# Optimization experiments

Hardware: AMD Instinct MI355X
Metric: run time of the kernel (lower is better)

Reference implementation:

```python
import jax, jax.numpy as jnp
import numpy as np

B, N, C, D = 4, 8192, 256, 256
WS = [2048, 4096, 8192]
RS = [1, 2, 4]
HEAD_IDX = 0


def setup_inputs() -> dict:
    key = jax.random.key(0)
    k1, k2, k3, k4 = jax.random.split(key, 4)
    scale = 1.0 / np.sqrt(C).astype(np.float32)
    x = jax.random.normal(k1, (B, N, C), jnp.float32)
    Wq = jax.random.normal(k2, (C, D), jnp.float32) * scale
    Wk = jax.random.normal(k3, (C, D), jnp.float32) * scale
    Wv = jax.random.normal(k4, (C, D), jnp.float32) * scale
    return {"x": x, "Wq": Wq, "Wk": Wk, "Wv": Wv}


def _causal_attn(v, Wq, Wk, Wv):
    # v: [Bseg, m, c] -> out [Bseg, m, D], denom [Bseg, m] (= sum_k exp(score))
    q = v @ Wq
    k = v @ Wk
    val = v @ Wv
    scores = jnp.einsum('bqd,bkd->bqk', q, k) / jnp.sqrt(jnp.asarray(D, v.dtype))
    m = v.shape[1]
    mask = jnp.tril(jnp.ones((m, m), bool))
    scores = jnp.where(mask, scores, -jnp.inf)
    mx = scores.max(-1)  # diagonal always unmasked -> finite
    e = jnp.exp(scores - mx[..., None])
    ssum = e.sum(-1)
    out = jnp.einsum('bqk,bkd->bqd', e, val) / ssum[..., None]
    denom = ssum * jnp.exp(mx)  # unnormalized softmax denominator
    return out, denom


def _dilated_forward(x, Wq, Wk, Wv):
    b, n, c = x.shape
    segs, idx_list = [], []
    for w, r in zip(WS, RS):
        off = HEAD_IDX % r
        s_cnt = n // w
        # [b, s, m, c] strided gather (offset::r within each window of size w)
        xr = x.reshape(b, s_cnt, w, c)[:, :, off::r, :]
        # segment-major then batch, matching torch.cat(..., dim=0) order
        segs.append(jnp.transpose(xr, (1, 0, 2, 3)).reshape(s_cnt * b, -1, c))
        pos = jnp.arange(off, w, r)
        idx_list.append(jnp.arange(s_cnt)[:, None] * w + pos[None, :])  # [s, m]
    batched = jnp.concatenate(segs, 0)  # [28, 2048, c]
    o_b, den_b = _causal_attn(batched, Wq, Wk, Wv)

    # per-token denominator sums across overlapping segments (scatter-add)
    sums = jnp.zeros((b, n), x.dtype)
    per_cfg = []
    start = 0
    for (w, r), idx in zip(zip(WS, RS), idx_list):
        s_cnt = n // w
        cnt = s_cnt * b
        o = jnp.transpose(o_b[start:start + cnt].reshape(s_cnt, b, -1, D), (1, 0, 2, 3))
        d = jnp.transpose(den_b[start:start + cnt].reshape(s_cnt, b, -1), (1, 0, 2))
        start += cnt
        flat_idx = idx.reshape(-1)  # [s*m]
        o_f = o.reshape(b, -1, D)
        d_f = d.reshape(b, -1)
        per_cfg.append((o_f, d_f, flat_idx))
        sums = sums.at[:, flat_idx].add(d_f)

    # weighted scatter-add of outputs, alpha = denom / denom_sum
    out = jnp.zeros((b, n, D), x.dtype)
    for o_f, d_f, flat_idx in per_cfg:
        alphas = d_f / sums[:, flat_idx]
        out = out.at[:, flat_idx, :].add(o_f * alphas[..., None])
    return out


def reference(x, Wq, Wk, Wv):
    return _dilated_forward(x, Wq, Wk, Wv)
```

## Files before the change

### kernel.cpp

```cpp
#include <hip/hip_runtime.h>
#include <hip/hip_bf16.h>

typedef __bf16 bf16;
typedef unsigned short u16;
typedef bf16 bf16x8 __attribute__((ext_vector_type(8)));
typedef bf16 bf16x2 __attribute__((ext_vector_type(2)));
typedef u16  u16x8  __attribute__((ext_vector_type(8)));
typedef u16  u16x4  __attribute__((ext_vector_type(4)));
typedef float f32x4 __attribute__((ext_vector_type(4)));
typedef float f32x16 __attribute__((ext_vector_type(16)));

#define MFMA16(a,b,c) __builtin_amdgcn_mfma_f32_16x16x32_bf16((a),(b),(c),0,0,0)
#define MFMA32(a,b,c) __builtin_amdgcn_mfma_f32_32x32x16_bf16((a),(b),(c),0,0,0)
#define QSCALE 0.09016844005625f

__device__ inline unsigned pack2(float a, float b) {
    bf16x2 t; t[0] = (bf16)a; t[1] = (bf16)b;
    return __builtin_bit_cast(unsigned, t);
}

__device__ __forceinline__ void load_lds16(const void* g, void* l) {
    __builtin_amdgcn_global_load_lds(
        (const __attribute__((address_space(1))) unsigned*)g,
        (__attribute__((address_space(3))) unsigned*)l, 16, 0, 0);
}

__device__ const unsigned short g_items[24] = {
    (unsigned short)(15 | (0u<<4) | (32u<<5)),
    (unsigned short)(14 | (0u<<4) | (32u<<5)),
    (unsigned short)(13 | (0u<<4) | (32u<<5)),
    (unsigned short)(12 | (0u<<4) | (32u<<5)),
    (unsigned short)(11 | (0u<<4) | (32u<<5)),
    (unsigned short)(10 | (0u<<4) | (32u<<5)),
    (unsigned short)( 9 | (0u<<4) | (32u<<5)),
    (unsigned short)( 8 | (0u<<4) | (32u<<5)),
    (unsigned short)(15 | (1u<<4) | (64u<<5)),
    (unsigned short)( 7 | (0u<<4) | (32u<<5)),
    (unsigned short)(14 | (1u<<4) | (60u<<5)),
    (unsigned short)( 6 | (0u<<4) | (28u<<5)),
    (unsigned short)(13 | (1u<<4) | (56u<<5)),
    (unsigned short)( 5 | (0u<<4) | (24u<<5)),
    (unsigned short)(12 | (1u<<4) | (52u<<5)),
    (unsigned short)( 4 | (0u<<4) | (20u<<5)),
    (unsigned short)(11 | (1u<<4) | (48u<<5)),
    (unsigned short)( 3 | (0u<<4) | (16u<<5)),
    (unsigned short)(10 | (1u<<4) | (44u<<5)),
    (unsigned short)( 2 | (0u<<4) | (12u<<5)),
    (unsigned short)( 9 | (1u<<4) | (40u<<5)),
    (unsigned short)( 1 | (0u<<4) | ( 8u<<5)),
    (unsigned short)( 8 | (1u<<4) | (36u<<5)),
    (unsigned short)( 0 | (0u<<4) | ( 4u<<5)),
};

__global__ void cvt_w(const float* __restrict__ Wq, const float* __restrict__ Wk,
                      const float* __restrict__ Wv, bf16* __restrict__ Wbt,
                      int* __restrict__ cnt) {
    if (blockIdx.x == 0 && threadIdx.x == 0) *cnt = 0;
    int idx = blockIdx.x * 256 + threadIdx.x;
    int which = idx >> 16;
    int rem = idx & 65535;
    int c = rem >> 8, d = rem & 255;
    const float* W = (which == 0) ? Wq : (which == 1) ? Wk : Wv;
    Wbt[(size_t)which * 65536 + d * 256 + c] = (bf16)W[c * 256 + d];
}

__global__ __launch_bounds__(256, 2)
void qkv_gemm(const float* __restrict__ x, const bf16* __restrict__ Wbt,
              bf16* __restrict__ Qb, bf16* __restrict__ Kb,
              bf16* __restrict__ Vtt1, bf16* __restrict__ Vtt2, bf16* __restrict__ Vtt4) {
    __shared__ __align__(16) u16 lA[64 * 136];
    __shared__ __align__(16) u16 lB[64 * 136];
    int mt = blockIdx.x;
    int tid = threadIdx.x, wv = tid >> 6, lane = tid & 63;
    int l15 = lane & 15, quad = lane >> 4;

    const float* Ax = x + (size_t)(mt * 64) * 256;
    int row = tid >> 2, c0 = (tid & 3) * 32;

    for (int which = 0; which < 3; which++) {
        f32x4 acc[4][4] = {};
        const bf16* Bw = Wbt + (size_t)which * 65536;

        for (int kh = 0; kh < 2; kh++) {
            __syncthreads();
            #pragma unroll
            for (int i = 0; i < 4; i++) {
                float4 f0 = *(const float4*)(Ax + row * 256 + kh * 128 + c0 + i * 8);
                float4 f1 = *(const float4*)(Ax + row * 256 + kh * 128 + c0 + i * 8 + 4);
                bf16x8 v;
                v[0] = (bf16)f0.x; v[1] = (bf16)f0.y; v[2] = (bf16)f0.z; v[3] = (bf16)f0.w;
                v[4] = (bf16)f1.x; v[5] = (bf16)f1.y; v[6] = (bf16)f1.z; v[7] = (bf16)f1.w;
                *(bf16x8*)((bf16*)lA + row * 136 + c0 + i * 8) = v;
            }
            for (int nt = 0; nt < 4; nt++) {
                __syncthreads();
                #pragma unroll
                for (int i = 0; i < 4; i++)
                    *(bf16x8*)((bf16*)lB + row * 136 + c0 + i * 8) =
                        *(const bf16x8*)(Bw + (size_t)(nt * 64 + row) * 256 + kh * 128 + c0 + i * 8);
                __syncthreads();
                #pragma unroll
                for (int ks = 0; ks < 4; ks++) {
                    bf16x8 a = *(const bf16x8*)((bf16*)lA + (wv * 16 + l15) * 136 + ks * 32 + quad * 8);
                    #pragma unroll
                    for (int ns = 0; ns < 4; ns++) {
                        bf16x8 b2 = *(const bf16x8*)((bf16*)lB + (ns * 16 + l15) * 136 + ks * 32 + quad * 8);
                        acc[nt][ns] = MFMA16(a, b2, acc[nt][ns]);
                    }
                }
            }
        }

        u16* lT = lA;
        float sc = (which == 0) ? QSCALE : 1.0f;
        for (int nt = 0; nt < 4; nt++) {
            __syncthreads();
            if (which < 2) {
                #pragma unroll
                for (int ns = 0; ns < 4; ns++)
                    #pragma unroll
                    for (int r = 0; r < 4; r++) {
                        bf16 v = (bf16)(acc[nt][ns][r] * sc);
                        lT[(wv * 16 + quad * 4 + r) * 72 + ns * 16 + l15] = *(u16*)&v;
                    }
                __syncthreads();
                bf16* outp = (which == 0) ? Qb : Kb;
                int tokl = tid >> 2, ch = tid & 3;
                u16x8 v0 = *(u16x8*)(lT + tokl * 72 + ch * 16);
                u16x8 v1 = *(u16x8*)(lT + tokl * 72 + ch * 16 + 8);
                u16* dst = (u16*)outp + (size_t)(mt * 64 + tokl) * 256 + nt * 64 + ch * 16;
                *(u16x8*)dst = v0;
                *(u16x8*)(dst + 8) = v1;
            } else {
                #pragma unroll
                for (int ns = 0; ns < 4; ns++)
                    #pragma unroll
                    for (int r = 0; r < 4; r++) {
                        bf16 v = (bf16)acc[nt][ns][r];
                        lT[(ns * 16 + l15) * 72 + wv * 16 + quad * 4 + r] = *(u16*)&v;
                    }
                __syncthreads();
                int gtok = mt * 64;
                int bL = gtok >> 13, n0 = gtok & 8191;
                int d_l = tid >> 2, q = tid & 3;
                int dg = nt * 64 + d_l;
                {
                    int s1 = n0 >> 11, j1 = n0 & 2047;
                    u16* dst = (u16*)Vtt1 + ((size_t)(bL * 4 + s1) * 64 + (j1 >> 5) + (q >> 1)) * 8192
                               + (size_t)dg * 32 + (q & 1) * 16;
                    u16x8 a0 = *(u16x8*)(lT + d_l * 72 + q * 16);
                    u16x8 a1 = *(u16x8*)(lT + d_l * 72 + q * 16 + 8);
                    *(u16x8*)dst = a0; *(u16x8*)(dst + 8) = a1;
                }
                {
                    int s2 = n0 >> 12, j2 = (n0 & 4095) >> 1;
                    u16x8 e;
                    #pragma unroll
                    for (int i = 0; i < 8; i++) e[i] = lT[d_l * 72 + q * 16 + 2 * i];
                    u16* dst = (u16*)Vtt2 + ((size_t)(bL * 2 + s2) * 64 + (j2 >> 5)) * 8192
                               + (size_t)dg * 32 + q * 8;
                    *(u16x8*)dst = e;
                }
                {
                    int j4 = n0 >> 2;
                    u16x4 e;
                    #pragma unroll
                    for (int i = 0; i < 4; i++) e[i] = lT[d_l * 72 + q * 16 + 4 * i];
                    u16* dst = (u16*)Vtt4 + ((size_t)bL * 64 + (j4 >> 5)) * 8192
                               + (size_t)dg * 32 + (j4 & 31) + q * 4;
                    *(u16x4*)dst = e;
                }
            }
        }
    }
}

__global__ __launch_bounds__(256, 2)
void attn(const bf16* __restrict__ Qb, const bf16* __restrict__ Kb,
          const bf16* __restrict__ Vtt1, const bf16* __restrict__ Vtt2,
          const bf16* __restrict__ Vtt4,
          float* __restrict__ O1, float* __restrict__ O2, float* __restrict__ O4,
          float* __restrict__ D1, float* __restrict__ D2, float* __restrict__ D4,
          float* __restrict__ PO, float* __restrict__ PD,
          int* __restrict__ cnt) {
    __shared__ __align__(16) char K_l[2][16384];
    __shared__ __align__(16) char V_l[2][16384];
    __shared__ int item_s;

    const int tid = threadIdx.x, wv = tid >> 6, lane = tid & 63;
    const int l31 = lane & 31, hi = lane >> 5;

    for (;;) {
        __syncthreads();
        if (tid == 0) item_s = atomicAdd(cnt, 1);
        __syncthreads();
        const int item = item_s;
        if (item >= 672) break;

        const unsigned e = g_items[item / 28];
        const int seg = item % 28;
        const int qt  = e & 15;
        const int ci  = (e >> 4) & 1;
        const int kt0 = ci << 5;
        const int kt1 = e >> 5;

        int lr, ss, b;
        if (seg < 16)      { lr = 0; ss = seg >> 2;        b = seg & 3;        }
        else if (seg < 24) { lr = 1; ss = (seg - 16) >> 2; b = (seg - 16) & 3; }
        else               { lr = 2; ss = 0;               b = seg - 24;       }
        const int rr = 1 << lr;
        const size_t base = (size_t)b * 8192 + (size_t)ss * (2048 << lr);
        const size_t pbase = (size_t)b * (8192 >> lr) + (size_t)ss * 2048;
        const int segi = (lr == 0) ? (b * 4 + ss) : (lr == 1) ? (b * 2 + ss) : b;
        const u16* Vseg = (const u16*)((lr == 0) ? Vtt1 : (lr == 1) ? Vtt2 : Vtt4)
                          + (size_t)segi * 524288;
        float* Op = (lr == 0) ? O1 : (lr == 1) ? O2 : O4;
        float* Dp = (lr == 0) ? D1 : (lr == 1) ? D2 : D4;

        const int ql = qt * 128 + wv * 32 + l31;
        const u16* Kp = (const u16*)Kb + base * 256;

        bf16x8 qf[16];
        {
            const bf16* qp = Qb + (base + (size_t)ql * rr) * 256 + hi * 8;
            #pragma unroll
            for (int ks = 0; ks < 16; ks++) qf[ks] = *(const bf16x8*)(qp + ks * 16);
        }

        auto stage = [&](int t, int bs) {
            #pragma unroll
            for (int i = 0; i < 4; i++) {
                const u16* src = Kp + (size_t)((t * 32 + (tid & 31)) * rr) * 256
                                 + (i * 8 + (tid >> 5)) * 8;
                load_lds16(src, &K_l[bs][i * 4096 + wv * 1024]);
            }
            #pragma unroll
            for (int i = 0; i < 4; i++) {
                const u16* src = Vseg + (size_t)t * 8192 + (size_t)tid * 32 + i * 8;
                load_lds16(src, &V_l[bs][i * 4096 + wv * 1024]);
            }
        };

        f32x16 o[8] = {};
        float m_run = -1e30f, l_run = 0.f;

        stage(kt0, 0);

        const int dtile = 4 * qt + wv;
        for (int kt = kt0; kt < kt1; kt++) {
            const int buf = (kt - kt0) & 1;
            asm volatile("s_waitcnt vmcnt(0)" ::: "memory");
            __builtin_amdgcn_s_barrier();
            __builtin_amdgcn_sched_barrier(0);
            if (kt + 1 < kt1) stage(kt + 1, buf ^ 1);

            if (kt <= dtile) {
                const char* Kbl = K_l[buf];
                const char* Vbl = V_l[buf];

                f32x16 sv = {};
                __builtin_amdgcn_s_setprio(1);
                #pragma unroll
                for (int ks = 0; ks < 16; ks++) {
                    bf16x8 kf = *(const bf16x8*)(Kbl + ks * 1024 + hi * 512 + l31 * 16);
                    sv = MFMA32(kf, qf[ks], sv);
                }
                __builtin_amdgcn_s_setprio(0);

                float mx = -1e30f;
                const bool diag = (kt == dtile);
                #pragma unroll
                for (int r = 0; r < 16; r++) {
                    float v = sv[r];
                    if (diag) {
                        int key = kt * 32 + (r & 3) + 8 * (r >> 2) + 4 * hi;
                        if (key > ql) v = -1e30f;
                        sv[r] = v;
                    }
                    mx = fmaxf(mx, v);
                }
                mx = fmaxf(mx, __shfl_xor(mx, 32));

                if (__any(mx > m_run + 12.0f)) {
                    float mnew = fmaxf(m_run, mx);
                    float fac = exp2f(m_run - mnew);
                    l_run *= fac;
                    #pragma unroll
                    for (int dg = 0; dg < 8; dg++)
                        #pragma unroll
                        for (int r = 0; r < 16; r++) o[dg][r] *= fac;
                    m_run = mnew;
                }

                float rs = 0.f;
                #pragma unroll
                for (int r = 0; r < 16; r++) {
                    float e2 = exp2f(sv[r] - m_run);
                    sv[r] = e2;
                    rs += e2;
                }
                rs += __shfl_xor(rs, 32);
                l_run += rs;

                unsigned pk[8];
                #pragma unroll
                for (int rq = 0; rq < 4; rq++) {
                    pk[2 * rq]     = pack2(sv[4 * rq],     sv[4 * rq + 1]);
                    pk[2 * rq + 1] = pack2(sv[4 * rq + 2], sv[4 * rq + 3]);
                }
                #pragma unroll
                for (int st = 0; st < 2; st++) {
                    unsigned p0 = pk[4 * st],     p1 = pk[4 * st + 1];
                    unsigned p2 = pk[4 * st + 2], p3 = pk[4 * st + 3];
                    unsigned s0 = (unsigned)__shfl_xor((int)p0, 32);
                    unsigned s1 = (unsigned)__shfl_xor((int)p1, 32);
                    unsigned s2 = (unsigned)__shfl_xor((int)p2, 32);
                    unsigned s3 = (unsigned)__shfl_xor((int)p3, 32);
                    union { unsigned u[4]; bf16x8 v; } pb;
                    pb.u[0] = hi ? s2 : p0;
                    pb.u[1] = hi ? s3 : p1;
                    pb.u[2] = hi ? p2 : s0;
                    pb.u[3] = hi ? p3 : s1;
                    __builtin_amdgcn_s_setprio(1);
                    #pragma unroll
                    for (int dg = 0; dg < 8; dg++) {
                        bf16x8 vf = *(const bf16x8*)(Vbl + (st * 2 + hi) * 4096 + dg * 512 + l31 * 16);
                        o[dg] = MFMA32(vf, pb.v, o[dg]);
                    }
                    __builtin_amdgcn_s_setprio(0);
                }
            }
        }

        float invl = 1.0f / l_run;
        size_t prow;
        float *obase, *dbase;
        if (ci == 0) { prow = pbase + (size_t)ql;                    obase = Op; dbase = Dp; }
        else         { prow = (size_t)seg * 1024 + (size_t)(ql - 1024); obase = PO; dbase = PD; }
        if (hi == 0) dbase[prow] = l_run * exp2f(m_run);
        float* orow = obase + prow * 256 + hi * 4;
        #pragma unroll
        for (int dg = 0; dg < 8; dg++)
            #pragma unroll
            for (int rq = 0; rq < 4; rq++) {
                f32x4 v;
                v[0] = o[dg][4 * rq]     * invl;
                v[1] = o[dg][4 * rq + 1] * invl;
                v[2] = o[dg][4 * rq + 2] * invl;
                v[3] = o[dg][4 * rq + 3] * invl;
                *(f32x4*)(orow + dg * 32 + rq * 8) = v;
            }
    }
}

__global__ void finalize(float* __restrict__ out, const float* __restrict__ O2,
                         const float* __restrict__ O4,
                         const float* __restrict__ D1, const float* __restrict__ D2,
                         const float* __restrict__ D4,
                         const float* __restrict__ PO, const float* __restrict__ PD) {
    int g = blockIdx.x * 256 + threadIdx.x;
    int t = g >> 6, dc = (g & 63) * 4;
    int b = t >> 13, n = t & 8191;
    float d1 = D1[t];
    float4 o1 = *(float4*)(out + (size_t)t * 256 + dc);
    float ax = o1.x * d1, ay = o1.y * d1, az = o1.z * d1, aw = o1.w * d1;
    float den = d1;
    {
        int j1 = n & 2047;
        if (j1 >= 1024) {
            size_t pp = (size_t)(4 * (n >> 11) + b) * 1024 + (j1 - 1024);
            float dp = PD[pp];
            const float4 op = *(const float4*)(PO + pp * 256 + dc);
            ax += op.x * dp; ay += op.y * dp; az += op.z * dp; aw += op.w * dp;
            den += dp;
        }
    }
    if ((n & 1) == 0) {
        int s2 = n >> 12, j2 = (n & 4095) >> 1;
        int pos2 = b * 4096 + s2 * 2048 + j2;
        float d2 = D2[pos2];
        const float4 o2 = *(const float4*)(O2 + (size_t)pos2 * 256 + dc);
        ax += o2.x * d2; ay += o2.y * d2; az += o2.z * d2; aw += o2.w * d2;
        den += d2;
        if (j2 >= 1024) {
            size_t pp = (size_t)(16 + 4 * s2 + b) * 1024 + (j2 - 1024);
            float dp = PD[pp];
            const float4 op = *(const float4*)(PO + pp * 256 + dc);
            ax += op.x * dp; ay += op.y * dp; az += op.z * dp; aw += op.w * dp;
            den += dp;
        }
    }
    if ((n & 3) == 0) {
        int j4 = n >> 2;
        int pos4 = b * 2048 + j4;
        float d4 = D4[pos4];
        const float4 o4 = *(const float4*)(O4 + (size_t)pos4 * 256 + dc);
        ax += o4.x * d4; ay += o4.y * d4; az += o4.z * d4; aw += o4.w * d4;
        den += d4;
        if (j4 >= 1024) {
            size_t pp = (size_t)(24 + b) * 1024 + (j4 - 1024);
            float dp = PD[pp];
            const float4 op = *(const float4*)(PO + pp * 256 + dc);
            ax += op.x * dp; ay += op.y * dp; az += op.z * dp; aw += op.w * dp;
            den += dp;
        }
    }
    float inv = 1.0f / den;
    float4 r; r.x = ax * inv; r.y = ay * inv; r.z = az * inv; r.w = aw * inv;
    *(float4*)(out + (size_t)t * 256 + dc) = r;
}

extern "C" void kernel_launch(void* const* d_in, const int* in_sizes, int n_in,
                              void* d_out, int out_size, void* d_ws, size_t ws_size,
                              hipStream_t stream) {
    const float* x  = (const float*)d_in[0];
    const float* Wq = (const float*)d_in[1];
    const float* Wk = (const float*)d_in[2];
    const float* Wv = (const float*)d_in[3];
    float* out = (float*)d_out;

    char* ws = (char*)d_ws;
    bf16* Qb   = (bf16*)(ws);
    bf16* Kb   = (bf16*)(ws + 16777216);
    bf16* Vtt1 = (bf16*)(ws + 33554432);
    bf16* Vtt2 = (bf16*)(ws + 50331648);
    bf16* Vtt4 = (bf16*)(ws + 58720256);
    bf16* Wbt  = (bf16*)(ws + 62914560);
    float* O2  = (float*)(ws + 63307776);
    float* O4  = (float*)(ws + 80084992);
    float* D1  = (float*)(ws + 88473600);
    float* D2  = (float*)(ws + 88604672);
    float* D4  = (float*)(ws + 88670208);
    int*   cnt = (int*)(ws + 88702976);
    float* PO  = (float*)(ws + 88703232);
    float* PD  = (float*)(ws + 118063360);

    cvt_w<<<768, 256, 0, stream>>>(Wq, Wk, Wv, Wbt, cnt);
    qkv_gemm<<<512, 256, 0, stream>>>(x, Wbt, Qb, Kb, Vtt1, Vtt2, Vtt4);
    attn<<<512, 256, 0, stream>>>(Qb, Kb, Vtt1, Vtt2, Vtt4, out, O2, O4,
                                  D1, D2, D4, PO, PD, cnt);
    finalize<<<8192, 256, 0, stream>>>(out, O2, O4, D1, D2, D4, PO, PD);
}
```

Before: 244.5 us.

## Read K and weight fragments directly from global memory instead of LDS staging

```diff
diff --git a/kernel.cpp b/kernel.cpp
--- a/kernel.cpp
+++ b/kernel.cpp
@@ -68,8 +68,8 @@
 void qkv_gemm(const float* __restrict__ x, const bf16* __restrict__ Wbt,
               bf16* __restrict__ Qb, bf16* __restrict__ Kb,
               bf16* __restrict__ Vtt1, bf16* __restrict__ Vtt2, bf16* __restrict__ Vtt4) {
-    __shared__ __align__(16) u16 lA[64 * 136];
-    __shared__ __align__(16) u16 lB[64 * 136];
+    __shared__ __align__(16) u16 lA[2][64 * 136];
+    __shared__ __align__(16) u16 lB[64 * 72];
     int mt = blockIdx.x;
     int tid = threadIdx.x, wv = tid >> 6, lane = tid & 63;
     int l15 = lane & 15, quad = lane >> 4;
@@ -77,41 +77,39 @@
     const float* Ax = x + (size_t)(mt * 64) * 256;
     int row = tid >> 2, c0 = (tid & 3) * 32;
 
+    #pragma unroll
+    for (int kh = 0; kh < 2; kh++)
+        #pragma unroll
+        for (int i = 0; i < 4; i++) {
+            float4 f0 = *(const float4*)(Ax + row * 256 + kh * 128 + c0 + i * 8);
+            float4 f1 = *(const float4*)(Ax + row * 256 + kh * 128 + c0 + i * 8 + 4);
+            bf16x8 v;
+            v[0] = (bf16)f0.x; v[1] = (bf16)f0.y; v[2] = (bf16)f0.z; v[3] = (bf16)f0.w;
+            v[4] = (bf16)f1.x; v[5] = (bf16)f1.y; v[6] = (bf16)f1.z; v[7] = (bf16)f1.w;
+            *(bf16x8*)((bf16*)lA[kh] + row * 136 + c0 + i * 8) = v;
+        }
+    __syncthreads();
+
     for (int which = 0; which < 3; which++) {
         f32x4 acc[4][4] = {};
         const bf16* Bw = Wbt + (size_t)which * 65536;
 
-        for (int kh = 0; kh < 2; kh++) {
-            __syncthreads();
+        #pragma unroll
+        for (int kh = 0; kh < 2; kh++)
             #pragma unroll
-            for (int i = 0; i < 4; i++) {
-                float4 f0 = *(const float4*)(Ax + row * 256 + kh * 128 + c0 + i * 8);
-                float4 f1 = *(const float4*)(Ax + row * 256 + kh * 128 + c0 + i * 8 + 4);
-                bf16x8 v;
-                v[0] = (bf16)f0.x; v[1] = (bf16)f0.y; v[2] = (bf16)f0.z; v[3] = (bf16)f0.w;
-                v[4] = (bf16)f1.x; v[5] = (bf16)f1.y; v[6] = (bf16)f1.z; v[7] = (bf16)f1.w;
-                *(bf16x8*)((bf16*)lA + row * 136 + c0 + i * 8) = v;
-            }
-            for (int nt = 0; nt < 4; nt++) {
-                __syncthreads();
-                #pragma unroll
-                for (int i = 0; i < 4; i++)
-                    *(bf16x8*)((bf16*)lB + row * 136 + c0 + i * 8) =
-                        *(const bf16x8*)(Bw + (size_t)(nt * 64 + row) * 256 + kh * 128 + c0 + i * 8);
-                __syncthreads();
-                #pragma unroll
-                for (int ks = 0; ks < 4; ks++) {
-                    bf16x8 a = *(const bf16x8*)((bf16*)lA + (wv * 16 + l15) * 136 + ks * 32 + quad * 8);
+            for (int ks = 0; ks < 4; ks++) {
+                bf16x8 a = *(const bf16x8*)((bf16*)lA[kh] + (wv * 16 + l15) * 136 + ks * 32 + quad * 8);
+                #pragma unroll
+                for (int nt = 0; nt < 4; nt++)
                     #pragma unroll
                     for (int ns = 0; ns < 4; ns++) {
-                        bf16x8 b2 = *(const bf16x8*)((bf16*)lB + (ns * 16 + l15) * 136 + ks * 32 + quad * 8);
+                        bf16x8 b2 = *(const bf16x8*)(Bw + (size_t)(nt * 64 + ns * 16 + l15) * 256
+                                                     + kh * 128 + ks * 32 + quad * 8);
                         acc[nt][ns] = MFMA16(a, b2, acc[nt][ns]);
                     }
-                }
             }
-        }
-
-        u16* lT = lA;
+
+        u16* lT = lB;
         float sc = (which == 0) ? QSCALE : 1.0f;
         for (int nt = 0; nt < 4; nt++) {
             __syncthreads();
@@ -183,7 +181,6 @@
           float* __restrict__ D1, float* __restrict__ D2, float* __restrict__ D4,
           float* __restrict__ PO, float* __restrict__ PD,
           int* __restrict__ cnt) {
-    __shared__ __align__(16) char K_l[2][16384];
     __shared__ __align__(16) char V_l[2][16384];
     __shared__ int item_s;
 
@@ -227,13 +224,7 @@
             for (int ks = 0; ks < 16; ks++) qf[ks] = *(const bf16x8*)(qp + ks * 16);
         }
 
-        auto stage = [&](int t, int bs) {
-            #pragma unroll
-            for (int i = 0; i < 4; i++) {
-                const u16* src = Kp + (size_t)((t * 32 + (tid & 31)) * rr) * 256
-                                 + (i * 8 + (tid >> 5)) * 8;
-                load_lds16(src, &K_l[bs][i * 4096 + wv * 1024]);
-            }
+        auto stageV = [&](int t, int bs) {
             #pragma unroll
             for (int i = 0; i < 4; i++) {
                 const u16* src = Vseg + (size_t)t * 8192 + (size_t)tid * 32 + i * 8;
@@ -244,7 +235,7 @@
         f32x16 o[8] = {};
         float m_run = -1e30f, l_run = 0.f;
 
-        stage(kt0, 0);
+        stageV(kt0, 0);
 
         const int dtile = 4 * qt + wv;
         for (int kt = kt0; kt < kt1; kt++) {
@@ -252,17 +243,17 @@
             asm volatile("s_waitcnt vmcnt(0)" ::: "memory");
             __builtin_amdgcn_s_barrier();
             __builtin_amdgcn_sched_barrier(0);
-            if (kt + 1 < kt1) stage(kt + 1, buf ^ 1);
+            if (kt + 1 < kt1) stageV(kt + 1, buf ^ 1);
 
             if (kt <= dtile) {
-                const char* Kbl = K_l[buf];
                 const char* Vbl = V_l[buf];
 
+                const bf16* krp = (const bf16*)(Kp + (size_t)((kt * 32 + l31) * rr) * 256 + hi * 8);
                 f32x16 sv = {};
                 __builtin_amdgcn_s_setprio(1);
                 #pragma unroll
                 for (int ks = 0; ks < 16; ks++) {
-                    bf16x8 kf = *(const bf16x8*)(Kbl + ks * 1024 + hi * 512 + l31 * 16);
+                    bf16x8 kf = *(const bf16x8*)(krp + ks * 16);
                     sv = MFMA32(kf, qf[ks], sv);
                 }
                 __builtin_amdgcn_s_setprio(0);
```

Measured after the change: 383.8 us. 57.0% more time.

## Static one-block-per-item attention grid and double-buffered weight staging in QKV GEMM

Applied to the files above, without the earlier changes.

```diff
diff --git a/kernel.cpp b/kernel.cpp
--- a/kernel.cpp
+++ b/kernel.cpp
@@ -53,9 +53,7 @@
 };
 
 __global__ void cvt_w(const float* __restrict__ Wq, const float* __restrict__ Wk,
-                      const float* __restrict__ Wv, bf16* __restrict__ Wbt,
-                      int* __restrict__ cnt) {
-    if (blockIdx.x == 0 && threadIdx.x == 0) *cnt = 0;
+                      const float* __restrict__ Wv, bf16* __restrict__ Wbt) {
     int idx = blockIdx.x * 256 + threadIdx.x;
     int which = idx >> 16;
     int rem = idx & 65535;
@@ -68,8 +66,9 @@
 void qkv_gemm(const float* __restrict__ x, const bf16* __restrict__ Wbt,
               bf16* __restrict__ Qb, bf16* __restrict__ Kb,
               bf16* __restrict__ Vtt1, bf16* __restrict__ Vtt2, bf16* __restrict__ Vtt4) {
-    __shared__ __align__(16) u16 lA[64 * 136];
-    __shared__ __align__(16) u16 lB[64 * 136];
+    __shared__ __align__(16) u16 lA[2][64 * 136];
+    __shared__ __align__(16) u16 lB[2][64 * 136];
+    __shared__ __align__(16) u16 lT[64 * 72];
     int mt = blockIdx.x;
     int tid = threadIdx.x, wv = tid >> 6, lane = tid & 63;
     int l15 = lane & 15, quad = lane >> 4;
@@ -77,41 +76,45 @@
     const float* Ax = x + (size_t)(mt * 64) * 256;
     int row = tid >> 2, c0 = (tid & 3) * 32;
 
+    #pragma unroll
+    for (int kh = 0; kh < 2; kh++)
+        #pragma unroll
+        for (int i = 0; i < 4; i++) {
+            float4 f0 = *(const float4*)(Ax + row * 256 + kh * 128 + c0 + i * 8);
+            float4 f1 = *(const float4*)(Ax + row * 256 + kh * 128 + c0 + i * 8 + 4);
+            bf16x8 v;
+            v[0] = (bf16)f0.x; v[1] = (bf16)f0.y; v[2] = (bf16)f0.z; v[3] = (bf16)f0.w;
+            v[4] = (bf16)f1.x; v[5] = (bf16)f1.y; v[6] = (bf16)f1.z; v[7] = (bf16)f1.w;
+            *(bf16x8*)((bf16*)lA[kh] + row * 136 + c0 + i * 8) = v;
+        }
+
+    auto stageW = [&](const bf16* Bw, int t, int bs) {
+        int kh = t >> 2, nt = t & 3;
+        #pragma unroll
+        for (int i = 0; i < 4; i++)
+            *(bf16x8*)((bf16*)lB[bs] + row * 136 + c0 + i * 8) =
+                *(const bf16x8*)(Bw + (size_t)(nt * 64 + row) * 256 + kh * 128 + c0 + i * 8);
+    };
+
     for (int which = 0; which < 3; which++) {
         f32x4 acc[4][4] = {};
         const bf16* Bw = Wbt + (size_t)which * 65536;
-
-        for (int kh = 0; kh < 2; kh++) {
+        stageW(Bw, 0, 0);
+        for (int t = 0; t < 8; t++) {
             __syncthreads();
-            #pragma unroll
-            for (int i = 0; i < 4; i++) {
-                float4 f0 = *(const float4*)(Ax + row * 256 + kh * 128 + c0 + i * 8);
-                float4 f1 = *(const float4*)(Ax + row * 256 + kh * 128 + c0 + i * 8 + 4);
-                bf16x8 v;
-                v[0] = (bf16)f0.x; v[1] = (bf16)f0.y; v[2] = (bf16)f0.z; v[3] = (bf16)f0.w;
-                v[4] = (bf16)f1.x; v[5] = (bf16)f1.y; v[6] = (bf16)f1.z; v[7] = (bf16)f1.w;
-                *(bf16x8*)((bf16*)lA + row * 136 + c0 + i * 8) = v;
-            }
-            for (int nt = 0; nt < 4; nt++) {
-                __syncthreads();
+            if (t + 1 < 8) stageW(Bw, t + 1, (t + 1) & 1);
+            int kh = t >> 2, nt = t & 3;
+            #pragma unroll
+            for (int ks = 0; ks < 4; ks++) {
+                bf16x8 a = *(const bf16x8*)((bf16*)lA[kh] + (wv * 16 + l15) * 136 + ks * 32 + quad * 8);
                 #pragma unroll
-                for (int i = 0; i < 4; i++)
-                    *(bf16x8*)((bf16*)lB + row * 136 + c0 + i * 8) =
-                        *(const bf16x8*)(Bw + (size_t)(nt * 64 + row) * 256 + kh * 128 + c0 + i * 8);
-                __syncthreads();
-                #pragma unroll
-                for (int ks = 0; ks < 4; ks++) {
-                    bf16x8 a = *(const bf16x8*)((bf16*)lA + (wv * 16 + l15) * 136 + ks * 32 + quad * 8);
-                    #pragma unroll
-                    for (int ns = 0; ns < 4; ns++) {
-                        bf16x8 b2 = *(const bf16x8*)((bf16*)lB + (ns * 16 + l15) * 136 + ks * 32 + quad * 8);
-                        acc[nt][ns] = MFMA16(a, b2, acc[nt][ns]);
-                    }
-                }
-            }
-        }
-
-        u16* lT = lA;
+                for (int ns = 0; ns < 4; ns++) {
+                    bf16x8 b2 = *(const bf16x8*)((bf16*)lB[t & 1] + (ns * 16 + l15) * 136 + ks * 32 + quad * 8);
+                    acc[nt][ns] = MFMA16(a, b2, acc[nt][ns]);
+                }
+            }
+        }
+
         float sc = (which == 0) ? QSCALE : 1.0f;
         for (int nt = 0; nt < 4; nt++) {
             __syncthreads();
@@ -181,176 +184,167 @@
           const bf16* __restrict__ Vtt4,
           float* __restrict__ O1, float* __restrict__ O2, float* __restrict__ O4,
           float* __restrict__ D1, float* __restrict__ D2, float* __restrict__ D4,
-          float* __restrict__ PO, float* __restrict__ PD,
-          int* __restrict__ cnt) {
+          float* __restrict__ PO, float* __restrict__ PD) {
     __shared__ __align__(16) char K_l[2][16384];
     __shared__ __align__(16) char V_l[2][16384];
-    __shared__ int item_s;
 
     const int tid = threadIdx.x, wv = tid >> 6, lane = tid & 63;
     const int l31 = lane & 31, hi = lane >> 5;
 
-    for (;;) {
-        __syncthreads();
-        if (tid == 0) item_s = atomicAdd(cnt, 1);
-        __syncthreads();
-        const int item = item_s;
-        if (item >= 672) break;
-
-        const unsigned e = g_items[item / 28];
-        const int seg = item % 28;
-        const int qt  = e & 15;
-        const int ci  = (e >> 4) & 1;
-        const int kt0 = ci << 5;
-        const int kt1 = e >> 5;
-
-        int lr, ss, b;
-        if (seg < 16)      { lr = 0; ss = seg >> 2;        b = seg & 3;        }
-        else if (seg < 24) { lr = 1; ss = (seg - 16) >> 2; b = (seg - 16) & 3; }
-        else               { lr = 2; ss = 0;               b = seg - 24;       }
-        const int rr = 1 << lr;
-        const size_t base = (size_t)b * 8192 + (size_t)ss * (2048 << lr);
-        const size_t pbase = (size_t)b * (8192 >> lr) + (size_t)ss * 2048;
-        const int segi = (lr == 0) ? (b * 4 + ss) : (lr == 1) ? (b * 2 + ss) : b;
-        const u16* Vseg = (const u16*)((lr == 0) ? Vtt1 : (lr == 1) ? Vtt2 : Vtt4)
-                          + (size_t)segi * 524288;
-        float* Op = (lr == 0) ? O1 : (lr == 1) ? O2 : O4;
-        float* Dp = (lr == 0) ? D1 : (lr == 1) ? D2 : D4;
-
-        const int ql = qt * 128 + wv * 32 + l31;
-        const u16* Kp = (const u16*)Kb + base * 256;
-
-        bf16x8 qf[16];
-        {
-            const bf16* qp = Qb + (base + (size_t)ql * rr) * 256 + hi * 8;
-            #pragma unroll
-            for (int ks = 0; ks < 16; ks++) qf[ks] = *(const bf16x8*)(qp + ks * 16);
-        }
-
-        auto stage = [&](int t, int bs) {
-            #pragma unroll
-            for (int i = 0; i < 4; i++) {
-                const u16* src = Kp + (size_t)((t * 32 + (tid & 31)) * rr) * 256
-                                 + (i * 8 + (tid >> 5)) * 8;
-                load_lds16(src, &K_l[bs][i * 4096 + wv * 1024]);
-            }
-            #pragma unroll
-            for (int i = 0; i < 4; i++) {
-                const u16* src = Vseg + (size_t)t * 8192 + (size_t)tid * 32 + i * 8;
-                load_lds16(src, &V_l[bs][i * 4096 + wv * 1024]);
-            }
-        };
-
-        f32x16 o[8] = {};
-        float m_run = -1e30f, l_run = 0.f;
-
-        stage(kt0, 0);
-
-        const int dtile = 4 * qt + wv;
-        for (int kt = kt0; kt < kt1; kt++) {
-            const int buf = (kt - kt0) & 1;
-            asm volatile("s_waitcnt vmcnt(0)" ::: "memory");
-            __builtin_amdgcn_s_barrier();
-            __builtin_amdgcn_sched_barrier(0);
-            if (kt + 1 < kt1) stage(kt + 1, buf ^ 1);
-
-            if (kt <= dtile) {
-                const char* Kbl = K_l[buf];
-                const char* Vbl = V_l[buf];
-
-                f32x16 sv = {};
+    const int item = (int)blockIdx.x;
+    const unsigned e = g_items[item / 28];
+    const int seg = item % 28;
+    const int qt  = e & 15;
+    const int ci  = (e >> 4) & 1;
+    const int kt0 = ci << 5;
+    const int kt1 = e >> 5;
+
+    int lr, ss, b;
+    if (seg < 16)      { lr = 0; ss = seg >> 2;        b = seg & 3;        }
+    else if (seg < 24) { lr = 1; ss = (seg - 16) >> 2; b = (seg - 16) & 3; }
+    else               { lr = 2; ss = 0;               b = seg - 24;       }
+    const int rr = 1 << lr;
+    const size_t base = (size_t)b * 8192 + (size_t)ss * (2048 << lr);
+    const size_t pbase = (size_t)b * (8192 >> lr) + (size_t)ss * 2048;
+    const int segi = (lr == 0) ? (b * 4 + ss) : (lr == 1) ? (b * 2 + ss) : b;
+    const u16* Vseg = (const u16*)((lr == 0) ? Vtt1 : (lr == 1) ? Vtt2 : Vtt4)
+                      + (size_t)segi * 524288;
+    float* Op = (lr == 0) ? O1 : (lr == 1) ? O2 : O4;
+    float* Dp = (lr == 0) ? D1 : (lr == 1) ? D2 : D4;
+
+    const int ql = qt * 128 + wv * 32 + l31;
+    const u16* Kp = (const u16*)Kb + base * 256;
+
+    bf16x8 qf[16];
+    {
+        const bf16* qp = Qb + (base + (size_t)ql * rr) * 256 + hi * 8;
+        #pragma unroll
+        for (int ks = 0; ks < 16; ks++) qf[ks] = *(const bf16x8*)(qp + ks * 16);
+    }
+
+    auto stage = [&](int t, int bs) {
+        #pragma unroll
+        for (int i = 0; i < 4; i++) {
+            const u16* src = Kp + (size_t)((t * 32 + (tid & 31)) * rr) * 256
+                             + (i * 8 + (tid >> 5)) * 8;
+            load_lds16(src, &K_l[bs][i * 4096 + wv * 1024]);
+        }
+        #pragma unroll
+        for (int i = 0; i < 4; i++) {
+            const u16* src = Vseg + (size_t)t * 8192 + (size_t)tid * 32 + i * 8;
+            load_lds16(src, &V_l[bs][i * 4096 + wv * 1024]);
+        }
+    };
+
+    f32x16 o[8] = {};
+    float m_run = -1e30f, l_run = 0.f;
+
+    stage(kt0, 0);
+
+    const int dtile = 4 * qt + wv;
+    for (int kt = kt0; kt < kt1; kt++) {
+        const int buf = (kt - kt0) & 1;
+        asm volatile("s_waitcnt vmcnt(0)" ::: "memory");
+        __builtin_amdgcn_s_barrier();
+        __builtin_amdgcn_sched_barrier(0);
+        if (kt + 1 < kt1) stage(kt + 1, buf ^ 1);
+
+        if (kt <= dtile) {
+            const char* Kbl = K_l[buf];
+            const char* Vbl = V_l[buf];
+
+            f32x16 sv = {};
+            __builtin_amdgcn_s_setprio(1);
+            #pragma unroll
+            for (int ks = 0; ks < 16; ks++) {
+                bf16x8 kf = *(const bf16x8*)(Kbl + ks * 1024 + hi * 512 + l31 * 16);
+                sv = MFMA32(kf, qf[ks], sv);
+            }
+            __builtin_amdgcn_s_setprio(0);
+
+            float mx = -1e30f;
+            const bool diag = (kt == dtile);
+            #pragma unroll
+            for (int r = 0; r < 16; r++) {
+                float v = sv[r];
+                if (diag) {
+                    int key = kt * 32 + (r & 3) + 8 * (r >> 2) + 4 * hi;
+                    if (key > ql) v = -1e30f;
+                    sv[r] = v;
+                }
+                mx = fmaxf(mx, v);
+            }
+            mx = fmaxf(mx, __shfl_xor(mx, 32));
+
+            if (__any(mx > m_run + 12.0f)) {
+                float mnew = fmaxf(m_run, mx);
+                float fac = exp2f(m_run - mnew);
+                l_run *= fac;
+                #pragma unroll
+                for (int dg = 0; dg < 8; dg++)
+                    #pragma unroll
+                    for (int r = 0; r < 16; r++) o[dg][r] *= fac;
+                m_run = mnew;
+            }
+
+            float rs = 0.f;
+            #pragma unroll
+            for (int r = 0; r < 16; r++) {
+                float e2 = exp2f(sv[r] - m_run);
+                sv[r] = e2;
+                rs += e2;
+            }
+            rs += __shfl_xor(rs, 32);
+            l_run += rs;
+
+            unsigned pk[8];
+            #pragma unroll
+            for (int rq = 0; rq < 4; rq++) {
+                pk[2 * rq]     = pack2(sv[4 * rq],     sv[4 * rq + 1]);
+                pk[2 * rq + 1] = pack2(sv[4 * rq + 2], sv[4 * rq + 3]);
+            }
+            #pragma unroll
+            for (int st = 0; st < 2; st++) {
+                unsigned p0 = pk[4 * st],     p1 = pk[4 * st + 1];
+                unsigned p2 = pk[4 * st + 2], p3 = pk[4 * st + 3];
+                unsigned s0 = (unsigned)__shfl_xor((int)p0, 32);
+                unsigned s1 = (unsigned)__shfl_xor((int)p1, 32);
+                unsigned s2 = (unsigned)__shfl_xor((int)p2, 32);
+                unsigned s3 = (unsigned)__shfl_xor((int)p3, 32);
+                union { unsigned u[4]; bf16x8 v; } pb;
+                pb.u[0] = hi ? s2 : p0;
+                pb.u[1] = hi ? s3 : p1;
+                pb.u[2] = hi ? p2 : s0;
+                pb.u[3] = hi ? p3 : s1;
                 __builtin_amdgcn_s_setprio(1);
                 #pragma unroll
-                for (int ks = 0; ks < 16; ks++) {
-                    bf16x8 kf = *(const bf16x8*)(Kbl + ks * 1024 + hi * 512 + l31 * 16);
-                    sv = MFMA32(kf, qf[ks], sv);
+                for (int dg = 0; dg < 8; dg++) {
+                    bf16x8 vf = *(const bf16x8*)(Vbl + (st * 2 + hi) * 4096 + dg * 512 + l31 * 16);
+                    o[dg] = MFMA32(vf, pb.v, o[dg]);
                 }
                 __builtin_amdgcn_s_setprio(0);
-
-                float mx = -1e30f;
-                const bool diag = (kt == dtile);
-                #pragma unroll
-                for (int r = 0; r < 16; r++) {
-                    float v = sv[r];
-                    if (diag) {
-                        int key = kt * 32 + (r & 3) + 8 * (r >> 2) + 4 * hi;
-                        if (key > ql) v = -1e30f;
-                        sv[r] = v;
-                    }
-                    mx = fmaxf(mx, v);
-                }
-                mx = fmaxf(mx, __shfl_xor(mx, 32));
-
-                if (__any(mx > m_run + 12.0f)) {
-                    float mnew = fmaxf(m_run, mx);
-                    float fac = exp2f(m_run - mnew);
-                    l_run *= fac;
-                    #pragma unroll
-                    for (int dg = 0; dg < 8; dg++)
-                        #pragma unroll
-                        for (int r = 0; r < 16; r++) o[dg][r] *= fac;
-                    m_run = mnew;
-                }
-
-                float rs = 0.f;
-                #pragma unroll
-                for (int r = 0; r < 16; r++) {
-                    float e2 = exp2f(sv[r] - m_run);
-                    sv[r] = e2;
-                    rs += e2;
-                }
-                rs += __shfl_xor(rs, 32);
-                l_run += rs;
-
-                unsigned pk[8];
-                #pragma unroll
-                for (int rq = 0; rq < 4; rq++) {
-                    pk[2 * rq]     = pack2(sv[4 * rq],     sv[4 * rq + 1]);
-                    pk[2 * rq + 1] = pack2(sv[4 * rq + 2], sv[4 * rq + 3]);
-                }
-                #pragma unroll
-                for (int st = 0; st < 2; st++) {
-                    unsigned p0 = pk[4 * st],     p1 = pk[4 * st + 1];
-                    unsigned p2 = pk[4 * st + 2], p3 = pk[4 * st + 3];
-                    unsigned s0 = (unsigned)__shfl_xor((int)p0, 32);
-                    unsigned s1 = (unsigned)__shfl_xor((int)p1, 32);
-                    unsigned s2 = (unsigned)__shfl_xor((int)p2, 32);
-                    unsigned s3 = (unsigned)__shfl_xor((int)p3, 32);
-                    union { unsigned u[4]; bf16x8 v; } pb;
-                    pb.u[0] = hi ? s2 : p0;
-                    pb.u[1] = hi ? s3 : p1;
-                    pb.u[2] = hi ? p2 : s0;
-                    pb.u[3] = hi ? p3 : s1;
-                    __builtin_amdgcn_s_setprio(1);
-                    #pragma unroll
-                    for (int dg = 0; dg < 8; dg++) {
-                        bf16x8 vf = *(const bf16x8*)(Vbl + (st * 2 + hi) * 4096 + dg * 512 + l31 * 16);
-                        o[dg] = MFMA32(vf, pb.v, o[dg]);
-                    }
-                    __builtin_amdgcn_s_setprio(0);
-                }
-            }
-        }
-
-        float invl = 1.0f / l_run;
-        size_t prow;
-        float *obase, *dbase;
-        if (ci == 0) { prow = pbase + (size_t)ql;                    obase = Op; dbase = Dp; }
-        else         { prow = (size_t)seg * 1024 + (size_t)(ql - 1024); obase = PO; dbase = PD; }
-        if (hi == 0) dbase[prow] = l_run * exp2f(m_run);
-        float* orow = obase + prow * 256 + hi * 4;
-        #pragma unroll
-        for (int dg = 0; dg < 8; dg++)
-            #pragma unroll
-            for (int rq = 0; rq < 4; rq++) {
-                f32x4 v;
-                v[0] = o[dg][4 * rq]     * invl;
-                v[1] = o[dg][4 * rq + 1] * invl;
-                v[2] = o[dg][4 * rq + 2] * invl;
-                v[3] = o[dg][4 * rq + 3] * invl;
-                *(f32x4*)(orow + dg * 32 + rq * 8) = v;
-            }
-    }
+            }
+        }
+    }
+
+    float invl = 1.0f / l_run;
+    size_t prow;
+    float *obase, *dbase;
+    if (ci == 0) { prow = pbase + (size_t)ql;                    obase = Op; dbase = Dp; }
+    else         { prow = (size_t)seg * 1024 + (size_t)(ql - 1024); obase = PO; dbase = PD; }
+    if (hi == 0) dbase[prow] = l_run * exp2f(m_run);
+    float* orow = obase + prow * 256 + hi * 4;
+    #pragma unroll
+    for (int dg = 0; dg < 8; dg++)
+        #pragma unroll
+        for (int rq = 0; rq < 4; rq++) {
+            f32x4 v;
+            v[0] = o[dg][4 * rq]     * invl;
+            v[1] = o[dg][4 * rq + 1] * invl;
+            v[2] = o[dg][4 * rq + 2] * invl;
+            v[3] = o[dg][4 * rq + 3] * invl;
+            *(f32x4*)(orow + dg * 32 + rq * 8) = v;
+        }
 }
 
 __global__ void finalize(float* __restrict__ out, const float* __restrict__ O2,
@@ -431,13 +425,12 @@
     float* D1  = (float*)(ws + 88473600);
     float* D2  = (float*)(ws + 88604672);
     float* D4  = (float*)(ws + 88670208);
-    int*   cnt = (int*)(ws + 88702976);
     float* PO  = (float*)(ws + 88703232);
     float* PD  = (float*)(ws + 118063360);
 
-    cvt_w<<<768, 256, 0, stream>>>(Wq, Wk, Wv, Wbt, cnt);
+    cvt_w<<<768, 256, 0, stream>>>(Wq, Wk, Wv, Wbt);
     qkv_gemm<<<512, 256, 0, stream>>>(x, Wbt, Qb, Kb, Vtt1, Vtt2, Vtt4);
-    attn<<<512, 256, 0, stream>>>(Qb, Kb, Vtt1, Vtt2, Vtt4, out, O2, O4,
-                                  D1, D2, D4, PO, PD, cnt);
+    attn<<<672, 256, 0, stream>>>(Qb, Kb, Vtt1, Vtt2, Vtt4, out, O2, O4,
+                                  D1, D2, D4, PO, PD);
     finalize<<<8192, 256, 0, stream>>>(out, O2, O4, D1, D2, D4, PO, PD);
 }
```

Result: faster. 236.7 us (-3.2%).
